# Kernel tuning notes

Measured on AMD Instinct MI355X. Metric: run time of the kernel, lower is better.

Reference implementation:

```python
import jax, jax.numpy as jnp
import numpy as np

N_HEADS = 16
HEAD_SIZE = 64
EMBED = 1024
BLOCK = 2048
B, T = 2, 2048


def setup_inputs() -> dict:
    key = jax.random.key(0)
    ks = jax.random.split(key, 6)
    scale = 0.02
    inputs = jax.random.normal(ks[0], (B, T, EMBED), dtype=jnp.float32)
    # per-head projection weights, stacked: [H, E, D]
    Wk = jax.random.normal(ks[1], (N_HEADS, EMBED, HEAD_SIZE), dtype=jnp.float32) * scale
    Wq = jax.random.normal(ks[2], (N_HEADS, EMBED, HEAD_SIZE), dtype=jnp.float32) * scale
    Wv = jax.random.normal(ks[3], (N_HEADS, EMBED, HEAD_SIZE), dtype=jnp.float32) * scale
    Wo = jax.random.normal(ks[4], (EMBED, EMBED), dtype=jnp.float32) * scale
    bo = jax.random.normal(ks[5], (EMBED,), dtype=jnp.float32) * scale
    return {"inputs": inputs, "Wk": Wk, "Wq": Wq, "Wv": Wv, "Wo": Wo, "bo": bo}


def reference(inputs, Wk, Wq, Wv, Wo, bo):
    # per-head projections: [B,H,T,D]
    k = jnp.einsum("bte,hed->bhtd", inputs, Wk)
    q = jnp.einsum("bte,hed->bhtd", inputs, Wq)
    v = jnp.einsum("bte,hed->bhtd", inputs, Wv)
    # NOTE: original computes wei = K @ Q^T (faithful reproduction)
    wei = jnp.einsum("bhtd,bhsd->bhts", k, q) * (HEAD_SIZE ** -0.5)
    causal = jnp.tril(jnp.ones((T, T), dtype=bool))  # tril==0 masked
    wei = jnp.where(causal, wei, -jnp.inf)
    wei = jax.nn.softmax(wei, axis=-1)
    out = jnp.einsum("bhts,bhsd->bhtd", wei, v)
    # concat heads along feature dim: [B,T,H*D]
    z = out.transpose(0, 2, 1, 3).reshape(B, T, N_HEADS * HEAD_SIZE)
    z = z @ Wo.T + bo  # match torch Linear(x) = x @ W^T + b
    return z
```

## Files before the change

kernel.cpp:

```cpp
#include <hip/hip_runtime.h>
#include <cstdint>
#include <cstddef>

typedef __bf16 bf8_t __attribute__((ext_vector_type(8)));
typedef float  f4_t  __attribute__((ext_vector_type(4)));

static __device__ __forceinline__ f4_t mfma16(bf8_t a, bf8_t b, f4_t c) {
    return __builtin_amdgcn_mfma_f32_16x16x32_bf16(a, b, c, 0, 0, 0);
}

#if defined(__has_builtin) && __has_builtin(__builtin_amdgcn_exp2f)
#define EXP2F(x) __builtin_amdgcn_exp2f(x)
#else
#define EXP2F(x) exp2f(x)
#endif

static __device__ __forceinline__ void async_ld16(const __bf16* g, __bf16* l) {
    __builtin_amdgcn_global_load_lds(
        (const __attribute__((address_space(1))) void*)(uintptr_t)g,
        (__attribute__((address_space(3))) void*)(uintptr_t)l, 16, 0, 0);
}


__global__ void __launch_bounds__(256) prep_convert(const float* __restrict__ X,
                                                    const float* __restrict__ Wo,
                                                    __bf16* __restrict__ Xbf,
                                                    __bf16* __restrict__ Wobf) {
    size_t bx = blockIdx.x;
    const float* src; __bf16* dst; size_t base;
    if (bx < 2048) { src = X;  dst = Xbf;  base = bx * 2048; }
    else           { src = Wo; dst = Wobf; base = (bx - 2048) * 2048; }
    size_t i = base + (size_t)threadIdx.x * 8;
    float4 a = *(const float4*)(src + i);
    float4 b = *(const float4*)(src + i + 4);
    bf8_t o;
    o[0] = (__bf16)a.x; o[1] = (__bf16)a.y; o[2] = (__bf16)a.z; o[3] = (__bf16)a.w;
    o[4] = (__bf16)b.x; o[5] = (__bf16)b.y; o[6] = (__bf16)b.z; o[7] = (__bf16)b.w;
    *(bf8_t*)(dst + i) = o;
}

__global__ void __launch_bounds__(256) wtrans(const float* __restrict__ Wq,
                                              const float* __restrict__ Wk,
                                              const float* __restrict__ Wv,
                                              __bf16* __restrict__ Wqt,
                                              __bf16* __restrict__ Wkt,
                                              __bf16* __restrict__ Wvt) {
    const float* W; __bf16* Wt;
    if (blockIdx.y == 0)      { W = Wq; Wt = Wqt; }
    else if (blockIdx.y == 1) { W = Wk; Wt = Wkt; }
    else                      { W = Wv; Wt = Wvt; }
    int h = blockIdx.x >> 4, eb = blockIdx.x & 15;
    __shared__ float tile[64][65];
    int tx = threadIdx.x;
    int e = tx >> 2, dg = (tx & 3) * 16;
    const float* src = W + ((size_t)h * 1024 + eb * 64 + e) * 64 + dg;
#pragma unroll
    for (int i = 0; i < 4; ++i) {
        float4 v = *(const float4*)(src + i * 4);
        tile[dg + i * 4 + 0][e] = v.x;
        tile[dg + i * 4 + 1][e] = v.y;
        tile[dg + i * 4 + 2][e] = v.z;
        tile[dg + i * 4 + 3][e] = v.w;
    }
    __syncthreads();
    int d = tx >> 2, eg = (tx & 3) * 16;
    __bf16* dst = Wt + (size_t)(h * 64 + d) * 1024 + eb * 64 + eg;
    bf8_t o0, o1;
#pragma unroll
    for (int i = 0; i < 8; ++i) o0[i] = (__bf16)tile[d][eg + i];
#pragma unroll
    for (int i = 0; i < 8; ++i) o1[i] = (__bf16)tile[d][eg + 8 + i];
    *(bf8_t*)dst       = o0;
    *(bf8_t*)(dst + 8) = o1;
}

static __device__ __forceinline__ void gemm_tile128(const __bf16* __restrict__ A,
                                                    const __bf16* __restrict__ Bt,
                                                    __bf16* As, __bf16* Bs,
                                                    int m0, int n0, f4_t acc[4][4]) {
    const int tid  = threadIdx.x;
    const int lane = tid & 63;
    const int wv   = tid >> 6;
    const int lrow = lane >> 3;
    const int lsc  = lane & 7;
    const int quad = lane >> 4;
    const int l15  = lane & 15;
    const int wm = (wv & 1) * 64;
    const int wn = (wv >> 1) * 64;
    f4_t zero = {0.f, 0.f, 0.f, 0.f};
#pragma unroll
    for (int mi = 0; mi < 4; ++mi)
#pragma unroll
        for (int ni = 0; ni < 4; ++ni) acc[mi][ni] = zero;

    for (int kb = 0; kb < 16; ++kb) {
#pragma unroll
        for (int j = 0; j < 4; ++j) {
            int row = wv * 32 + j * 8 + lrow;
            int lc  = lsc ^ (row & 7);
            async_ld16(A + (size_t)(m0 + row) * 1024 + kb * 64 + lc * 8,
                       As + (wv * 32 + j * 8) * 64);
            async_ld16(Bt + (size_t)(n0 + row) * 1024 + kb * 64 + lc * 8,
                       Bs + (wv * 32 + j * 8) * 64);
        }
        __syncthreads();
#pragma unroll
        for (int ks = 0; ks < 2; ++ks) {
            bf8_t af[4], bfr[4];
#pragma unroll
            for (int mi = 0; mi < 4; ++mi) {
                int row = wm + mi * 16 + l15;
                int ch  = (ks * 4 + quad) ^ (row & 7);
                af[mi] = *(const bf8_t*)(As + row * 64 + ch * 8);
            }
#pragma unroll
            for (int ni = 0; ni < 4; ++ni) {
                int row = wn + ni * 16 + l15;
                int ch  = (ks * 4 + quad) ^ (row & 7);
                bfr[ni] = *(const bf8_t*)(Bs + row * 64 + ch * 8);
            }
#pragma unroll
            for (int mi = 0; mi < 4; ++mi)
#pragma unroll
                for (int ni = 0; ni < 4; ++ni)
                    acc[mi][ni] = mfma16(af[mi], bfr[ni], acc[mi][ni]);
        }
        __syncthreads();
    }
}

__global__ void __launch_bounds__(256) gemm_proj(const __bf16* __restrict__ Xbf,
                                                 const __bf16* __restrict__ Wqt,
                                                 const __bf16* __restrict__ Wkt,
                                                 const __bf16* __restrict__ Wvt,
                                                 __bf16* __restrict__ Qb,
                                                 __bf16* __restrict__ Kb,
                                                 __bf16* __restrict__ Vt) {
    __shared__ __bf16 smem[17408];
    __bf16* As = smem;
    __bf16* Bs = smem + 8192;
    int which = blockIdx.y;
    const __bf16* Bt = which == 0 ? Wqt : (which == 1 ? Wkt : Wvt);
    int m0 = ((int)blockIdx.x >> 3) * 128;
    int n0 = ((int)blockIdx.x & 7) * 128;
    f4_t acc[4][4];
    gemm_tile128(Xbf, Bt, As, Bs, m0, n0, acc);
    const int lane = threadIdx.x & 63, wv = threadIdx.x >> 6;
    const int quad = lane >> 4, l15 = lane & 15;
    const int wm = (wv & 1) * 64, wn = (wv >> 1) * 64;
    if (which < 2) {
        __bf16* C = which ? Kb : Qb;
        const float scl = which ? 0.18033688f : 1.0f;
#pragma unroll
        for (int mi = 0; mi < 4; ++mi)
#pragma unroll
            for (int ni = 0; ni < 4; ++ni)
#pragma unroll
                for (int r = 0; r < 4; ++r) {
                    int m = m0 + wm + mi * 16 + quad * 4 + r;
                    int n = n0 + wn + ni * 16 + l15;
                    int b = m >> 11, t = m & 2047;
                    int h = n >> 6,  d = n & 63;
                    C[((size_t)(b * 16 + h) * 2048 + t) * 64 + d] = (__bf16)(acc[mi][ni][r] * scl);
                }
    } else {
        const int STR = 136;
#pragma unroll
        for (int mi = 0; mi < 4; ++mi)
#pragma unroll
            for (int ni = 0; ni < 4; ++ni)
#pragma unroll
                for (int r = 0; r < 4; ++r) {
                    int ml = wm + mi * 16 + quad * 4 + r;
                    int nl = wn + ni * 16 + l15;
                    smem[nl * STR + ml] = (__bf16)acc[mi][ni][r];
                }
        __syncthreads();
        int b = m0 >> 11, tg0 = m0 & 2047;
        int nl = (int)threadIdx.x >> 1;
        int tc = ((int)threadIdx.x & 1) * 64;
        int n = n0 + nl, h = n >> 6, d = n & 63;
        __bf16* dst = Vt + ((size_t)(b * 16 + h) * 64 + d) * 2048 + tg0 + tc;
        const __bf16* srcl = smem + nl * STR + tc;
#pragma unroll
        for (int k = 0; k < 8; ++k)
            *(bf8_t*)(dst + k * 8) = *(const bf8_t*)(srcl + k * 8);
    }
}

static __device__ __forceinline__ void gemm_tile(const __bf16* __restrict__ A,
                                                 const __bf16* __restrict__ Bt,
                                                 __bf16* As, __bf16* Bs,
                                                 int m0, int n0, f4_t acc[4][2]) {
    const int tid  = threadIdx.x;
    const int lane = tid & 63;
    const int wv   = tid >> 6;
    const int lrow = lane >> 3;
    const int lsc  = lane & 7;
    const int quad = lane >> 4;
    const int l15  = lane & 15;
    const int wm = (wv & 1) * 64;
    const int wn = (wv >> 1) * 32;
    f4_t zero = {0.f, 0.f, 0.f, 0.f};
#pragma unroll
    for (int mi = 0; mi < 4; ++mi)
#pragma unroll
        for (int ni = 0; ni < 2; ++ni) acc[mi][ni] = zero;

    for (int kb = 0; kb < 16; ++kb) {
#pragma unroll
        for (int j = 0; j < 4; ++j) {
            int row = wv * 32 + j * 8 + lrow;
            int lc  = lsc ^ (row & 7);
            async_ld16(A + (size_t)(m0 + row) * 1024 + kb * 64 + lc * 8,
                       As + (wv * 32 + j * 8) * 64);
        }
#pragma unroll
        for (int j = 0; j < 2; ++j) {
            int row = wv * 16 + j * 8 + lrow;
            int lc  = lsc ^ (row & 7);
            async_ld16(Bt + (size_t)(n0 + row) * 1024 + kb * 64 + lc * 8,
                       Bs + (wv * 16 + j * 8) * 64);
        }
        __syncthreads();
#pragma unroll
        for (int ks = 0; ks < 2; ++ks) {
            bf8_t af[4], bfr[2];
#pragma unroll
            for (int mi = 0; mi < 4; ++mi) {
                int row = wm + mi * 16 + l15;
                int ch  = (ks * 4 + quad) ^ (row & 7);
                af[mi] = *(const bf8_t*)(As + row * 64 + ch * 8);
            }
#pragma unroll
            for (int ni = 0; ni < 2; ++ni) {
                int row = wn + ni * 16 + l15;
                int ch  = (ks * 4 + quad) ^ (row & 7);
                bfr[ni] = *(const bf8_t*)(Bs + row * 64 + ch * 8);
            }
#pragma unroll
            for (int mi = 0; mi < 4; ++mi)
#pragma unroll
                for (int ni = 0; ni < 2; ++ni)
                    acc[mi][ni] = mfma16(af[mi], bfr[ni], acc[mi][ni]);
        }
        __syncthreads();
    }
}

__global__ void __launch_bounds__(256) gemm_out(const __bf16* __restrict__ Ob,
                                                const __bf16* __restrict__ Wobf,
                                                const float* __restrict__ bo,
                                                float* __restrict__ out) {
    __shared__ __bf16 smem[128 * 64 + 64 * 64];
    __bf16* As = smem;
    __bf16* Bs = smem + 128 * 64;
    int m0 = ((int)blockIdx.x >> 4) * 128;
    int n0 = ((int)blockIdx.x & 15) * 64;
    f4_t acc[4][2];
    gemm_tile(Ob, Wobf, As, Bs, m0, n0, acc);
    const int lane = threadIdx.x & 63, wv = threadIdx.x >> 6;
    const int quad = lane >> 4, l15 = lane & 15;
    const int wm = (wv & 1) * 64, wn = (wv >> 1) * 32;
#pragma unroll
    for (int mi = 0; mi < 4; ++mi)
#pragma unroll
        for (int ni = 0; ni < 2; ++ni)
#pragma unroll
            for (int r = 0; r < 4; ++r) {
                int m = m0 + wm + mi * 16 + quad * 4 + r;
                int n = n0 + wn + ni * 16 + l15;
                out[(size_t)m * 1024 + n] = acc[mi][ni][r] + bo[n];
            }
}

__global__ void __launch_bounds__(256, 2) attn(const __bf16* __restrict__ Kb,
                                               const __bf16* __restrict__ Qb,
                                               const __bf16* __restrict__ Vt,
                                               __bf16* __restrict__ Ob,
                                               int* __restrict__ ctrs) {
    __shared__ __bf16 Qs[2][64 * 64];
    __shared__ __bf16 Vs[2][64 * 64];
    __shared__ __bf16 Ps[4][16 * 72];
    __shared__ int item_lds;
    const int tid = threadIdx.x, lane = tid & 63, wv = tid >> 6;
    const int quad = lane >> 4, l15 = lane & 15;
    const int lrow8 = lane >> 3, lchunk = lane & 7;
    int xcc;
    asm volatile("s_getreg_b32 %0, hwreg(HW_REG_XCC_ID)" : "=s"(xcc));
    xcc &= 7;
    int* ctr = ctrs + xcc * 16;
    __bf16* Psw = &Ps[wv][0];
    f4_t zero = {0.f, 0.f, 0.f, 0.f};

    for (;;) {
        if (tid == 0) item_lds = atomicAdd(ctr, 1);
        __syncthreads();
        const int q = item_lds;
        if (q >= 128) break;
        const int tt = 31 - (q >> 2);
        const int bh = xcc * 4 + (q & 3);
        const int b = bh >> 4, h = bh & 15;
        const int t0 = tt * 64;
        const int tw = t0 + wv * 16;
        const __bf16* Kp = Kb + (size_t)bh * 2048 * 64;
        const __bf16* Qp = Qb + (size_t)bh * 2048 * 64;
        const __bf16* Vp = Vt + (size_t)bh * 64 * 2048;

        bf8_t kfrag[2];
#pragma unroll
        for (int ks = 0; ks < 2; ++ks)
            kfrag[ks] = *(const bf8_t*)(Kp + (size_t)(tw + l15) * 64 + ks * 32 + quad * 8);

        f4_t oacc[4];
#pragma unroll
        for (int ni = 0; ni < 4; ++ni) oacc[ni] = zero;
        float lsum[4] = {0.f, 0.f, 0.f, 0.f};

        auto stage = [&](int buf, int s0) {
#pragma unroll
            for (int j = 0; j < 2; ++j) {
                int row = wv * 8 + j * 32 + lrow8;
                int cg  = lchunk ^ (row & 7);
                async_ld16(Qp + (size_t)(s0 + row) * 64 + cg * 8,
                           &Qs[buf][(wv * 8 + j * 32) * 64]);
                async_ld16(Vp + (size_t)row * 2048 + s0 + cg * 8,
                           &Vs[buf][(wv * 8 + j * 32) * 64]);
            }
        };

        const int nsb = tt + 1;
        stage(0, 0);
        for (int sb = 0; sb < nsb; ++sb) {
            const int cur = sb & 1;
            const int s0 = sb * 64;
            const bool masked = (sb == nsb - 1);
            __syncthreads();
            if (sb + 1 < nsb) stage(1 ^ cur, s0 + 64);
            const __bf16* Qc = &Qs[cur][0];
            const __bf16* Vc = &Vs[cur][0];
            f4_t sacc[4] = {zero, zero, zero, zero};
#pragma unroll
            for (int ks = 0; ks < 2; ++ks) {
                bf8_t qf[4];
#pragma unroll
                for (int st = 0; st < 4; ++st) {
                    int row = st * 16 + l15;
                    int ch  = (ks * 4 + quad) ^ (row & 7);
                    qf[st] = *(const bf8_t*)(Qc + row * 64 + ch * 8);
                }
#pragma unroll
                for (int st = 0; st < 4; ++st)
                    sacc[st] = mfma16(kfrag[ks], qf[st], sacc[st]);
            }
#pragma unroll
            for (int st = 0; st < 4; ++st)
#pragma unroll
                for (int r = 0; r < 4; ++r) {
                    float e = EXP2F(sacc[st][r]);
                    if (masked && (s0 + st * 16 + l15 > tw + quad * 4 + r)) e = 0.0f;
                    lsum[r] += e;
                    Psw[(quad * 4 + r) * 72 + st * 16 + l15] = (__bf16)e;
                }
            asm volatile("s_waitcnt lgkmcnt(0)" ::: "memory");
            bf8_t pf[2];
#pragma unroll
            for (int ks = 0; ks < 2; ++ks)
                pf[ks] = *(const bf8_t*)(Psw + l15 * 72 + ks * 32 + quad * 8);
#pragma unroll
            for (int ks = 0; ks < 2; ++ks) {
                bf8_t vf[4];
#pragma unroll
                for (int ni = 0; ni < 4; ++ni) {
                    int row = ni * 16 + l15;
                    int ch  = (ks * 4 + quad) ^ (row & 7);
                    vf[ni] = *(const bf8_t*)(Vc + row * 64 + ch * 8);
                }
#pragma unroll
                for (int ni = 0; ni < 4; ++ni)
                    oacc[ni] = mfma16(pf[ks], vf[ni], oacc[ni]);
            }
        }

#pragma unroll
        for (int r = 0; r < 4; ++r) {
            float l = lsum[r];
            l += __shfl_xor(l, 1);
            l += __shfl_xor(l, 2);
            l += __shfl_xor(l, 4);
            l += __shfl_xor(l, 8);
            float inv = 1.0f / l;
            int t = tw + quad * 4 + r;
#pragma unroll
            for (int ni = 0; ni < 4; ++ni)
                Ob[((size_t)(b * 2048 + t) * 16 + h) * 64 + ni * 16 + l15] =
                    (__bf16)(oacc[ni][r] * inv);
        }
    }
}

extern "C" void kernel_launch(void* const* d_in, const int* in_sizes, int n_in,
                              void* d_out, int out_size, void* d_ws, size_t ws_size,
                              hipStream_t stream) {
    const float* X  = (const float*)d_in[0];
    const float* Wk = (const float*)d_in[1];
    const float* Wq = (const float*)d_in[2];
    const float* Wv = (const float*)d_in[3];
    const float* Wo = (const float*)d_in[4];
    const float* bo = (const float*)d_in[5];
    float* out = (float*)d_out;

    __bf16* ws   = (__bf16*)d_ws;
    __bf16* Xbf  = ws;
    __bf16* Wqt  = ws + 4194304;
    __bf16* Wkt  = ws + 5242880;
    __bf16* Wvt  = ws + 6291456;
    __bf16* Wobf = ws + 7340032;
    __bf16* Qb   = ws + 8388608;
    __bf16* Kb   = ws + 12582912;
    __bf16* Vt   = ws + 16777216;
    __bf16* Ob   = ws + 20971520;
    int* ctrs = (int*)d_ws;

    prep_convert<<<2560, 256, 0, stream>>>(X, Wo, Xbf, Wobf);
    wtrans<<<dim3(256, 3), 256, 0, stream>>>(Wq, Wk, Wv, Wqt, Wkt, Wvt);
    gemm_proj<<<dim3(256, 3), 256, 0, stream>>>(Xbf, Wqt, Wkt, Wvt, Qb, Kb, Vt);
    hipMemsetAsync(ctrs, 0, 512, stream);
    attn<<<512, 256, 0, stream>>>(Kb, Qb, Vt, Ob, ctrs);
    gemm_out<<<512, 256, 0, stream>>>(Ob, Wobf, bo, out);
}
```

Before: 189.3 us.

## Merge prep kernels, stage Q/K stores via LDS, raise attention occupancy

```diff
diff --git a/kernel.cpp b/kernel.cpp
--- a/kernel.cpp
+++ b/kernel.cpp
@@ -22,35 +22,38 @@
 }
 
 
-__global__ void __launch_bounds__(256) prep_convert(const float* __restrict__ X,
-                                                    const float* __restrict__ Wo,
-                                                    __bf16* __restrict__ Xbf,
-                                                    __bf16* __restrict__ Wobf) {
-    size_t bx = blockIdx.x;
-    const float* src; __bf16* dst; size_t base;
-    if (bx < 2048) { src = X;  dst = Xbf;  base = bx * 2048; }
-    else           { src = Wo; dst = Wobf; base = (bx - 2048) * 2048; }
-    size_t i = base + (size_t)threadIdx.x * 8;
-    float4 a = *(const float4*)(src + i);
-    float4 b = *(const float4*)(src + i + 4);
-    bf8_t o;
-    o[0] = (__bf16)a.x; o[1] = (__bf16)a.y; o[2] = (__bf16)a.z; o[3] = (__bf16)a.w;
-    o[4] = (__bf16)b.x; o[5] = (__bf16)b.y; o[6] = (__bf16)b.z; o[7] = (__bf16)b.w;
-    *(bf8_t*)(dst + i) = o;
-}
-
-__global__ void __launch_bounds__(256) wtrans(const float* __restrict__ Wq,
-                                              const float* __restrict__ Wk,
-                                              const float* __restrict__ Wv,
-                                              __bf16* __restrict__ Wqt,
-                                              __bf16* __restrict__ Wkt,
-                                              __bf16* __restrict__ Wvt) {
+__global__ void __launch_bounds__(256) prep_all(const float* __restrict__ X,
+                                                const float* __restrict__ Wo,
+                                                const float* __restrict__ Wq,
+                                                const float* __restrict__ Wk,
+                                                const float* __restrict__ Wv,
+                                                __bf16* __restrict__ Xbf,
+                                                __bf16* __restrict__ Wobf,
+                                                __bf16* __restrict__ Wqt,
+                                                __bf16* __restrict__ Wkt,
+                                                __bf16* __restrict__ Wvt) {
+    __shared__ float tile[64][65];
+    int bx = (int)blockIdx.x;
+    if (bx < 2560) {
+        const float* src; __bf16* dst; size_t base;
+        if (bx < 2048) { src = X;  dst = Xbf;  base = (size_t)bx * 2048; }
+        else           { src = Wo; dst = Wobf; base = (size_t)(bx - 2048) * 2048; }
+        size_t i = base + (size_t)threadIdx.x * 8;
+        float4 a = *(const float4*)(src + i);
+        float4 b = *(const float4*)(src + i + 4);
+        bf8_t o;
+        o[0] = (__bf16)a.x; o[1] = (__bf16)a.y; o[2] = (__bf16)a.z; o[3] = (__bf16)a.w;
+        o[4] = (__bf16)b.x; o[5] = (__bf16)b.y; o[6] = (__bf16)b.z; o[7] = (__bf16)b.w;
+        *(bf8_t*)(dst + i) = o;
+        return;
+    }
+    int wt = bx - 2560;
+    int which = wt >> 8, inner = wt & 255;
     const float* W; __bf16* Wt;
-    if (blockIdx.y == 0)      { W = Wq; Wt = Wqt; }
-    else if (blockIdx.y == 1) { W = Wk; Wt = Wkt; }
-    else                      { W = Wv; Wt = Wvt; }
-    int h = blockIdx.x >> 4, eb = blockIdx.x & 15;
-    __shared__ float tile[64][65];
+    if (which == 0)      { W = Wq; Wt = Wqt; }
+    else if (which == 1) { W = Wk; Wt = Wkt; }
+    else                 { W = Wv; Wt = Wvt; }
+    int h = inner >> 4, eb = inner & 15;
     int tx = threadIdx.x;
     int e = tx >> 2, dg = (tx & 3) * 16;
     const float* src = W + ((size_t)h * 1024 + eb * 64 + e) * 64 + dg;
@@ -129,13 +132,13 @@
     }
 }
 
-__global__ void __launch_bounds__(256) gemm_proj(const __bf16* __restrict__ Xbf,
-                                                 const __bf16* __restrict__ Wqt,
-                                                 const __bf16* __restrict__ Wkt,
-                                                 const __bf16* __restrict__ Wvt,
-                                                 __bf16* __restrict__ Qb,
-                                                 __bf16* __restrict__ Kb,
-                                                 __bf16* __restrict__ Vt) {
+__global__ void __launch_bounds__(256, 3) gemm_proj(const __bf16* __restrict__ Xbf,
+                                                    const __bf16* __restrict__ Wqt,
+                                                    const __bf16* __restrict__ Wkt,
+                                                    const __bf16* __restrict__ Wvt,
+                                                    __bf16* __restrict__ Qb,
+                                                    __bf16* __restrict__ Kb,
+                                                    __bf16* __restrict__ Vt) {
     __shared__ __bf16 smem[17408];
     __bf16* As = smem;
     __bf16* Bs = smem + 8192;
@@ -148,6 +151,7 @@
     const int lane = threadIdx.x & 63, wv = threadIdx.x >> 6;
     const int quad = lane >> 4, l15 = lane & 15;
     const int wm = (wv & 1) * 64, wn = (wv >> 1) * 64;
+    const int STR = 136;
     if (which < 2) {
         __bf16* C = which ? Kb : Qb;
         const float scl = which ? 0.18033688f : 1.0f;
@@ -157,14 +161,22 @@
             for (int ni = 0; ni < 4; ++ni)
 #pragma unroll
                 for (int r = 0; r < 4; ++r) {
-                    int m = m0 + wm + mi * 16 + quad * 4 + r;
-                    int n = n0 + wn + ni * 16 + l15;
-                    int b = m >> 11, t = m & 2047;
-                    int h = n >> 6,  d = n & 63;
-                    C[((size_t)(b * 16 + h) * 2048 + t) * 64 + d] = (__bf16)(acc[mi][ni][r] * scl);
+                    int ml = wm + mi * 16 + quad * 4 + r;
+                    int nl = wn + ni * 16 + l15;
+                    smem[ml * STR + nl] = (__bf16)(acc[mi][ni][r] * scl);
                 }
+        __syncthreads();
+        int row = (int)threadIdx.x >> 1;
+        int seg = (int)threadIdx.x & 1;
+        int m = m0 + row;
+        int b = m >> 11, t = m & 2047;
+        int h = (n0 >> 6) + seg;
+        __bf16* dst = C + ((size_t)(b * 16 + h) * 2048 + t) * 64;
+        const __bf16* srcl = smem + row * STR + seg * 64;
+#pragma unroll
+        for (int k = 0; k < 8; ++k)
+            *(bf8_t*)(dst + k * 8) = *(const bf8_t*)(srcl + k * 8);
     } else {
-        const int STR = 136;
 #pragma unroll
         for (int mi = 0; mi < 4; ++mi)
 #pragma unroll
@@ -274,7 +286,7 @@
             }
 }
 
-__global__ void __launch_bounds__(256, 2) attn(const __bf16* __restrict__ Kb,
+__global__ void __launch_bounds__(256, 3) attn(const __bf16* __restrict__ Kb,
                                                const __bf16* __restrict__ Qb,
                                                const __bf16* __restrict__ Vt,
                                                __bf16* __restrict__ Ob,
@@ -422,10 +434,9 @@
     __bf16* Ob   = ws + 20971520;
     int* ctrs = (int*)d_ws;
 
-    prep_convert<<<2560, 256, 0, stream>>>(X, Wo, Xbf, Wobf);
-    wtrans<<<dim3(256, 3), 256, 0, stream>>>(Wq, Wk, Wv, Wqt, Wkt, Wvt);
+    prep_all<<<3328, 256, 0, stream>>>(X, Wo, Wq, Wk, Wv, Xbf, Wobf, Wqt, Wkt, Wvt);
     gemm_proj<<<dim3(256, 3), 256, 0, stream>>>(Xbf, Wqt, Wkt, Wvt, Qb, Kb, Vt);
     hipMemsetAsync(ctrs, 0, 512, stream);
-    attn<<<512, 256, 0, stream>>>(Kb, Qb, Vt, Ob, ctrs);
+    attn<<<768, 256, 0, stream>>>(Kb, Qb, Vt, Ob, ctrs);
     gemm_out<<<512, 256, 0, stream>>>(Ob, Wobf, bo, out);
 }
```

Result: faster. 171.9 us (-9.2%).
